# Kernel optimization log

Measured on AMD Instinct MI355X. Metric: run time of the kernel, lower is better.

## Reference

```python
import jax, jax.numpy as jnp
import numpy as np
from jax import lax


def setup_inputs() -> dict:
    key = jax.random.key(0)
    k1, k2, k3 = jax.random.split(key, 3)
    B, H, W_, C = 2, 384, 1280, 3
    F = 32
    return {
        "xl": jax.random.normal(k1, (B, H, W_, C), dtype=jnp.float32),
        "xr": jax.random.normal(k2, (B, H, W_, C), dtype=jnp.float32),
        "W": jax.random.normal(k3, (3, 3, C, F), dtype=jnp.float32) * 0.1,
        "b": jnp.zeros((F,), dtype=jnp.float32),
        "num_disparity": 96,
    }


def _features(x, W, b):
    # stand-in for the pretrained backbone: 3x3 stride-2 conv + relu (channels_last)
    f = lax.conv_general_dilated(x, W, window_strides=(2, 2), padding="SAME",
                                 dimension_numbers=("NHWC", "HWIO", "NHWC"))
    return jax.nn.relu(f + b)


def reference(xl, xr, W, b, num_disparity):
    D = num_disparity
    x = jnp.concatenate([xl, xr], axis=0)            # [2B,H,W,3]
    f = _features(x, W, b)                            # [2B,H/2,W/2,F]
    f = jax.image.resize(f, (f.shape[0], f.shape[1] * 2, f.shape[2] * 2, f.shape[3]),
                         method="bilinear")          # [2B,H,W,F]
    fl, fr = jnp.split(f, 2, axis=0)                  # each [B,H,W,F]

    # plane-sweep cost volume: sum over channels of squared diff vs width-rolled right features
    def step(_, d):
        cost_d = jnp.sum((fl - jnp.roll(fr, d, axis=2)) ** 2, axis=-1)  # [B,H,W]
        return None, cost_d

    _, cost = lax.scan(step, None, jnp.arange(D))     # [D,B,H,W]

    s = -177.0 * cost / jnp.max(cost, axis=0, keepdims=True)
    w = jax.nn.softmax(s, axis=0)
    disp_idx = jnp.arange(D, dtype=w.dtype)[:, None, None, None]
    return jnp.sum(disp_idx * w, axis=0)              # [B,H,W]
```

## Files before the change

### kernel.cpp

```cpp
#include <hip/hip_runtime.h>
#include <cstddef>

typedef _Float16 h2    __attribute__((ext_vector_type(2)));
typedef _Float16 half8 __attribute__((ext_vector_type(8)));
typedef float    f32x4 __attribute__((ext_vector_type(4)));
typedef float    f32x2 __attribute__((ext_vector_type(2)));

#define CH    192
#define CWID  640
#define IMG_H 384
#define IMG_W 1280
#define TW    128
#define GR    224
#define RAWC  179
#define RAWP  192

__device__ __forceinline__ float fastrcp(float x) {
#if __has_builtin(__builtin_amdgcn_rcpf)
  return __builtin_amdgcn_rcpf(x);
#else
  return 1.0f / x;
#endif
}
__device__ __forceinline__ float fastexp2(float x) {
#if __has_builtin(__builtin_amdgcn_exp2f)
  return __builtin_amdgcn_exp2f(x);
#else
  return exp2f(x);
#endif
}
__device__ __forceinline__ f32x2 xsw16(float x) {
#if __has_builtin(__builtin_amdgcn_permlane16_swap)
  auto r = __builtin_amdgcn_permlane16_swap(__float_as_uint(x), __float_as_uint(x), false, false);
  f32x2 o; o.x = __uint_as_float(r[0]); o.y = __uint_as_float(r[1]); return o;
#else
  f32x2 o; o.x = x;
  o.y = __uint_as_float((unsigned)__builtin_amdgcn_ds_swizzle((int)__float_as_uint(x), 0x401F));
  return o;
#endif
}
__device__ __forceinline__ f32x2 xsw32(float x) {
#if __has_builtin(__builtin_amdgcn_permlane32_swap)
  auto r = __builtin_amdgcn_permlane32_swap(__float_as_uint(x), __float_as_uint(x), false, false);
  f32x2 o; o.x = __uint_as_float(r[0]); o.y = __uint_as_float(r[1]); return o;
#else
  const int bpa = ((threadIdx.x & 63) ^ 32) << 2;
  f32x2 o; o.x = x;
  o.y = __uint_as_float((unsigned)__builtin_amdgcn_ds_bpermute(bpa, (int)__float_as_uint(x)));
  return o;
#endif
}
__device__ __forceinline__ f32x2 pkadd(f32x2 a, f32x2 b) {
  f32x2 d; asm("v_pk_add_f32 %0, %1, %2" : "=v"(d) : "v"(a), "v"(b)); return d;
}
__device__ __forceinline__ f32x2 pkfma(f32x2 a, f32x2 b, f32x2 c) {
  f32x2 d; asm("v_pk_fma_f32 %0, %1, %2, %3" : "=v"(d) : "v"(a), "v"(b), "v"(c)); return d;
}
__device__ __forceinline__ float min3f(float a, float b, float c) {
  float d; asm("v_min3_f32 %0, %1, %2, %3" : "=v"(d) : "v"(a), "v"(b), "v"(c)); return d;
}
__device__ __forceinline__ float max3f(float a, float b, float c) {
  float d; asm("v_max3_f32 %0, %1, %2, %3" : "=v"(d) : "v"(a), "v"(b), "v"(c)); return d;
}
__device__ __forceinline__ f32x2 lo2(f32x4 v) { f32x2 r; r.x = v.x; r.y = v.y; return r; }
__device__ __forceinline__ f32x2 hi2(f32x4 v) { f32x2 r; r.x = v.z; r.y = v.w; return r; }

__global__ __launch_bounds__(256)
void conv_relu_kernel(const float* __restrict__ xl, const float* __restrict__ xr,
                      const float* __restrict__ Wt, const float* __restrict__ bias,
                      _Float16* __restrict__ Fc) {
  __shared__ float wl[864];
  __shared__ float bl[32];
  const int tid = threadIdx.x;
  for (int t = tid; t < 864; t += 256) wl[t] = Wt[t];
  if (tid < 32) bl[tid] = bias[tid];
  __syncthreads();

  const int g  = blockIdx.x * 256 + tid;
  const int ow = g % CWID;
  const int t2 = g / CWID;
  const int oh = t2 % CH;
  const int bb = t2 / CH;
  const float* src = (bb < 2) ? (xl + (size_t)bb * IMG_H * IMG_W * 3)
                              : (xr + (size_t)(bb - 2) * IMG_H * IMG_W * 3);
  float acc[32];
  #pragma unroll
  for (int c = 0; c < 32; ++c) acc[c] = bl[c];

  #pragma unroll
  for (int kh = 0; kh < 3; ++kh) {
    const int ir = oh * 2 + kh;
    if (ir >= IMG_H) continue;
    #pragma unroll
    for (int kw = 0; kw < 3; ++kw) {
      const int ic = ow * 2 + kw;
      if (ic >= IMG_W) continue;
      const float* px = src + ((size_t)ir * IMG_W + ic) * 3;
      #pragma unroll
      for (int ci = 0; ci < 3; ++ci) {
        const float v = px[ci];
        const float* wp = &wl[((kh * 3 + kw) * 3 + ci) * 32];
        #pragma unroll
        for (int c8 = 0; c8 < 8; ++c8) {
          const float4 w4 = *(const float4*)(wp + c8 * 4);
          acc[c8 * 4 + 0] = fmaf(v, w4.x, acc[c8 * 4 + 0]);
          acc[c8 * 4 + 1] = fmaf(v, w4.y, acc[c8 * 4 + 1]);
          acc[c8 * 4 + 2] = fmaf(v, w4.z, acc[c8 * 4 + 2]);
          acc[c8 * 4 + 3] = fmaf(v, w4.w, acc[c8 * 4 + 3]);
        }
      }
    }
  }
  _Float16 hv[32];
  #pragma unroll
  for (int c = 0; c < 32; ++c) hv[c] = (_Float16)fmaxf(acc[c], 0.f);
  half8* dst = (half8*)(Fc + (size_t)g * 32);
  #pragma unroll
  for (int q = 0; q < 4; ++q) {
    half8 o;
    #pragma unroll
    for (int e = 0; e < 8; ++e) o[e] = hv[q * 8 + e];
    dst[q] = o;
  }
}

__global__ __launch_bounds__(256, 4)
void disparity_mfma_kernel(const _Float16* __restrict__ Fc, float* __restrict__ out) {
  __shared__ alignas(16) _Float16 raw[RAWP * 16];
  __shared__ alignas(16) _Float16 flH[8 * 512];
  __shared__ alignas(16) _Float16 gH[14 * 512];
  __shared__ alignas(16) float As[TW];
  __shared__ alignas(16) float Bs[GR];

  const int tid = threadIdx.x;
  const int w0  = blockIdx.x * TW;
  const int h   = blockIdx.y;
  const int bz  = blockIdx.z;

  const int hk = h >> 1;
  int r0, r1; float wv0;
  if (h & 1) { r0 = hk; r1 = (hk + 1 > CH - 1) ? CH - 1 : hk + 1; wv0 = 0.75f; }
  else       { r0 = (hk - 1 < 0) ? 0 : hk - 1; r1 = hk;           wv0 = 0.25f; }
  const half8 w0v = (half8)(_Float16)wv0;
  const half8 w1v = (half8)(_Float16)(1.0f - wv0);

  const int vbaseL = (w0 >> 1) + 639;
  const int vbaseR = (w0 >> 1) + 592;

  char* const rawB = (char*)raw;

  const char* const bL0 = (const char*)(Fc + ((size_t)bz * CH + r0) * CWID * 32);
  const char* const bL1 = (const char*)(Fc + ((size_t)bz * CH + r1) * CWID * 32);
  const char* const bR0 = (const char*)(Fc + ((size_t)(bz + 2) * CH + r0) * CWID * 32);
  const char* const bR1 = (const char*)(Fc + ((size_t)(bz + 2) * CH + r1) * CWID * 32);

  const _Float16 h75 = (_Float16)0.75f, h25 = (_Float16)0.25f;
  int a_r0off, a_s0, a_r1off, a_s1, a_swz; half8 a_h0, a_h1; char* a_dst;
  int b_r0off, b_s0, b_r1off, b_s1, b_swz; half8 b_h0, b_h1; char* b_dst;
  {
    const int row = tid;
    const bool isfl = row < TW;
    const int r  = isfl ? row : row - TW;
    const int uv = isfl ? (w0 + r) : (w0 - 95 + r);
    const int uact = uv < 0 ? uv + IMG_W : (uv >= IMG_W ? uv - IMG_W : uv);
    const int up = uv + IMG_W;
    const int vm0 = (up - 1) >> 1;
    int t0 = vm0 - (isfl ? vbaseL : (vbaseR - 66));
    int t1 = t0 + 1;
    if (uact == 0)         t0 = t1;
    if (uact == IMG_W - 1) t1 = t0;
    a_h0 = (half8)((up & 1) ? h75 : h25);
    a_h1 = (half8)((up & 1) ? h25 : h75);
    a_r0off = t0 * 32; a_s0 = (t0 & 1) << 4;
    a_r1off = t1 * 32; a_s1 = (t1 & 1) << 4;
    a_swz = (r >> 1) & 3;
    a_dst = (char*)(isfl ? flH : gH) + (r >> 4) * 1024 + (r & 15) * 64;
  }
  {
    const int row = tid + 256;
    const int r  = row - TW;
    const int uv = w0 - 95 + r;
    const int uact = uv < 0 ? uv + IMG_W : (uv >= IMG_W ? uv - IMG_W : uv);
    const int up = uv + IMG_W;
    const int vm0 = (up - 1) >> 1;
    int t0 = vm0 - (vbaseR - 66);
    int t1 = t0 + 1;
    if (uact == 0)         t0 = t1;
    if (uact == IMG_W - 1) t1 = t0;
    b_h0 = (half8)((up & 1) ? h75 : h25);
    b_h1 = (half8)((up & 1) ? h25 : h75);
    b_r0off = t0 * 32; b_s0 = (t0 & 1) << 4;
    b_r1off = t1 * 32; b_s1 = (t1 & 1) << 4;
    b_swz = (r >> 1) & 3;
    b_dst = (char*)gH + (r >> 4) * 1024 + (r & 15) * 64;
  }

  float sA = 0.f, sB = 0.f;
  #pragma unroll
  for (int half = 0; half < 2; ++half) {
    #pragma unroll
    for (int it = 0; it < 2; ++it) {
      const int task = tid + it * 256;
      if (it == 0 || tid < 128) {
        const int t    = task >> 1;
        const int cpos = task & 1;
        const int tc   = (t > RAWC - 1) ? RAWC - 1 : t;
        const bool isfl = tc < 66;
        int v = isfl ? (vbaseL + tc) : (vbaseR + tc - 66);
        v -= (v >= 640) ? 640 : 0;
        v -= (v >= 640) ? 640 : 0;
        const char* p0 = isfl ? bL0 : bR0;
        const char* p1 = isfl ? bL1 : bR1;
        const int off = (v << 6) + ((half * 2 + cpos) << 4);
        const half8 a0 = *(const half8*)(p0 + off);
        const half8 a1 = *(const half8*)(p1 + off);
        const half8 vv = a0 * w0v + a1 * w1v;
        *(half8*)(rawB + t * 32 + ((cpos ^ (t & 1)) << 4)) = vv;
      }
    }
    __syncthreads();

    #pragma unroll
    for (int cpos = 0; cpos < 2; ++cpos) {
      const int c16 = half * 2 + cpos;
      const int cb  = cpos << 4;
      {
        const half8 a = *(const half8*)(rawB + a_r0off + (cb ^ a_s0));
        const half8 b = *(const half8*)(rawB + a_r1off + (cb ^ a_s1));
        const half8 v = a * a_h0 + b * a_h1;
        #pragma unroll
        for (int e = 0; e < 4; ++e) {
          h2 pe = {v[2 * e], v[2 * e + 1]};
#if __has_builtin(__builtin_amdgcn_fdot2)
          sA = __builtin_amdgcn_fdot2(pe, pe, sA, false);
#else
          sA += (float)pe[0] * (float)pe[0] + (float)pe[1] * (float)pe[1];
#endif
        }
        *(half8*)(a_dst + ((c16 ^ a_swz) << 4)) = v;
      }
      if (tid < TW + GR - 256) {
        const half8 a = *(const half8*)(rawB + b_r0off + (cb ^ b_s0));
        const half8 b = *(const half8*)(rawB + b_r1off + (cb ^ b_s1));
        const half8 v = a * b_h0 + b * b_h1;
        #pragma unroll
        for (int e = 0; e < 4; ++e) {
          h2 pe = {v[2 * e], v[2 * e + 1]};
#if __has_builtin(__builtin_amdgcn_fdot2)
          sB = __builtin_amdgcn_fdot2(pe, pe, sB, false);
#else
          sB += (float)pe[0] * (float)pe[0] + (float)pe[1] * (float)pe[1];
#endif
        }
        *(half8*)(b_dst + ((c16 ^ b_swz) << 4)) = v;
      }
    }
    __syncthreads();
  }
  if (tid < TW) As[tid] = sA; else Bs[tid - TW] = sA;
  if (tid < TW + GR - 256) Bs[tid + 256 - TW] = sB;
  __syncthreads();

  const int lane = tid & 63;
  const int wid  = tid >> 6;
  const int n  = lane & 15;
  const int gq = lane >> 4;
  const int foffB = n * 64 + ((gq ^ ((n >> 1) & 3)) << 4);
  const float Cbase = (float)(95 - 4 * gq + n);

  const int mmb = gq * 4;
  const bool s0 = (mmb + 0) >= n, s1 = (mmb + 1) >= n;
  const bool s2 = (mmb + 2) >= n, s3 = (mmb + 3) >= n;
  const float kf0 = s0 ? 0.f : 96.f;
  const float kf1 = s1 ? 1.f : 97.f;
  const float kf2 = s2 ? 2.f : 98.f;
  const float kf3 = s3 ? 3.f : 99.f;

  #pragma unroll
  for (int pp = 0; pp < 2; ++pp) {
    const int p = wid * 2 + pp;
    const half8 bfrag = *(const half8*)((const char*)flH + p * 1024 + foffB);
    f32x4 acc[7];
    #pragma unroll
    for (int dq = 0; dq < 7; ++dq) {
      const half8 afrag = *(const half8*)((const char*)gH + (p + dq) * 1024 + foffB);
      f32x4 z = {0.f, 0.f, 0.f, 0.f};
      acc[dq] = __builtin_amdgcn_mfma_f32_16x16x32_f16(afrag, bfrag, z, 0, 0, 0);
    }

    const float Ai = As[p * 16 + n];
    const f32x4 b40 = *(const f32x4*)(&Bs[p * 16 + mmb]);
    const f32x4 b46 = *(const f32x4*)(&Bs[(p + 6) * 16 + mmb]);
    const float cm0 = fmaf(-2.f, s0 ? acc[0].x : acc[6].x, Ai + (s0 ? b40.x : b46.x));
    const float cm1 = fmaf(-2.f, s1 ? acc[0].y : acc[6].y, Ai + (s1 ? b40.y : b46.y));
    const float cm2 = fmaf(-2.f, s2 ? acc[0].z : acc[6].z, Ai + (s2 ? b40.z : b46.z));
    const float cm3 = fmaf(-2.f, s3 ? acc[0].w : acc[6].w, Ai + (s3 ? b40.w : b46.w));
    float mn = min3f(fminf(cm0, cm1), cm2, cm3);
    float mx = max3f(fmaxf(cm0, cm1), cm2, cm3);

    f32x2 AiP; AiP.x = Ai; AiP.y = Ai;
    f32x2 m2P; m2P.x = -2.f; m2P.y = -2.f;
    #pragma unroll
    for (int dq = 1; dq < 6; ++dq) {
      const f32x4 b4 = *(const f32x4*)(&Bs[(p + dq) * 16 + mmb]);
      const f32x2 c01 = pkfma(m2P, lo2(acc[dq]), pkadd(AiP, lo2(b4)));
      const f32x2 c23 = pkfma(m2P, hi2(acc[dq]), pkadd(AiP, hi2(b4)));
      mn = min3f(mn, c01.x, c01.y);
      mn = min3f(mn, c23.x, c23.y);
      mx = max3f(mx, c01.x, c01.y);
      mx = max3f(mx, c23.x, c23.y);
      acc[dq].x = c01.x; acc[dq].y = c01.y;
      acc[dq].z = c23.x; acc[dq].w = c23.y;
    }
    f32x2 t;
    t = xsw16(mn); mn = fminf(t.x, t.y);
    t = xsw32(mn); mn = fminf(t.x, t.y);
    t = xsw16(mx); mx = fmaxf(t.x, t.y);
    t = xsw32(mx); mx = fmaxf(t.x, t.y);

    const float ralpha = 177.0f * 1.4426950408889634f * fastrcp(mx);
    const float na   = -ralpha;
    const float base = ralpha * mn;
    f32x2 naP;   naP.x = na;   naP.y = na;
    f32x2 baseP; baseP.x = base; baseP.y = base;
    const float w0_ = fastexp2(fmaf(na, cm0, base));
    const float w1_ = fastexp2(fmaf(na, cm1, base));
    const float w2_ = fastexp2(fmaf(na, cm2, base));
    const float w3_ = fastexp2(fmaf(na, cm3, base));
    float sw0 = w0_, sw1 = w1_, sw2 = w2_, sw3 = w3_;
    float sk0 = kf0 * w0_;
    float sk1 = kf1 * w1_;
    float sk2 = kf2 * w2_;
    float sk3 = kf3 * w3_;
    #pragma unroll
    for (int dq = 1; dq < 6; ++dq) {
      const f32x2 g01 = pkfma(naP, lo2(acc[dq]), baseP);
      const f32x2 g23 = pkfma(naP, hi2(acc[dq]), baseP);
      const float u0 = fastexp2(g01.x);
      const float u1 = fastexp2(g01.y);
      const float u2 = fastexp2(g23.x);
      const float u3 = fastexp2(g23.y);
      sw0 += u0; sw1 += u1; sw2 += u2; sw3 += u3;
      sk0 = fmaf((float)(16 * dq + 0), u0, sk0);
      sk1 = fmaf((float)(16 * dq + 1), u1, sk1);
      sk2 = fmaf((float)(16 * dq + 2), u2, sk2);
      sk3 = fmaf((float)(16 * dq + 3), u3, sk3);
    }
    float sw  = (sw0 + sw1) + (sw2 + sw3);
    float skw = (sk0 + sk1) + (sk2 + sk3);
    float sdw = fmaf(Cbase, sw, -skw);
    t = xsw16(sw);  sw  = t.x + t.y;
    t = xsw16(sdw); sdw = t.x + t.y;
    t = xsw32(sw);  sw  = t.x + t.y;
    t = xsw32(sdw); sdw = t.x + t.y;
    if (gq == 0)
      out[((size_t)bz * IMG_H + h) * IMG_W + w0 + p * 16 + n] = sdw * fastrcp(sw);
  }
}

extern "C" void kernel_launch(void* const* d_in, const int* in_sizes, int n_in,
                              void* d_out, int out_size, void* d_ws, size_t ws_size,
                              hipStream_t stream) {
  (void)in_sizes; (void)n_in; (void)out_size; (void)ws_size;
  const float* xl   = (const float*)d_in[0];
  const float* xr   = (const float*)d_in[1];
  const float* Wt   = (const float*)d_in[2];
  const float* bias = (const float*)d_in[3];
  _Float16* Fc = (_Float16*)d_ws;
  float* out = (float*)d_out;

  hipLaunchKernelGGL(conv_relu_kernel, dim3(1920), dim3(256), 0, stream,
                     xl, xr, Wt, bias, Fc);
  hipLaunchKernelGGL(disparity_mfma_kernel, dim3(IMG_W / TW, IMG_H, 2), dim3(256), 0, stream,
                     Fc, out);
}
```

Baseline: 73.60 us.

## Move backbone conv to split-fp16 MFMA with LDS-staged input tiles

The scalar per-pixel 3x3 stride-2 conv is replaced by a tiled kernel. It stages five input rows in LDS, builds an im2col patch matrix with K=27 padded to 32, and computes it with 16x16x32 fp16 MFMAs. Precision is kept with a hi/lo fp16 split (three MFMAs per tile). The disparity kernel also drops the per-row Ai addition from every cost candidate and folds it into the max normalisation instead, since min and argmin shift uniformly. This costs extra LDS, swizzled layouts and split-precision work for the conv.

```diff
diff --git a/kernel.cpp b/kernel.cpp
--- a/kernel.cpp
+++ b/kernel.cpp
@@ -2,6 +2,7 @@
 #include <cstddef>
 
 typedef _Float16 h2    __attribute__((ext_vector_type(2)));
+typedef _Float16 half4 __attribute__((ext_vector_type(4)));
 typedef _Float16 half8 __attribute__((ext_vector_type(8)));
 typedef float    f32x4 __attribute__((ext_vector_type(4)));
 typedef float    f32x2 __attribute__((ext_vector_type(2)));
@@ -50,9 +51,6 @@
   return o;
 #endif
 }
-__device__ __forceinline__ f32x2 pkadd(f32x2 a, f32x2 b) {
-  f32x2 d; asm("v_pk_add_f32 %0, %1, %2" : "=v"(d) : "v"(a), "v"(b)); return d;
-}
 __device__ __forceinline__ f32x2 pkfma(f32x2 a, f32x2 b, f32x2 c) {
   f32x2 d; asm("v_pk_fma_f32 %0, %1, %2, %3" : "=v"(d) : "v"(a), "v"(b), "v"(c)); return d;
 }
@@ -66,61 +64,143 @@
 __device__ __forceinline__ f32x2 hi2(f32x4 v) { f32x2 r; r.x = v.z; r.y = v.w; return r; }
 
 __global__ __launch_bounds__(256)
-void conv_relu_kernel(const float* __restrict__ xl, const float* __restrict__ xr,
+void conv_mfma_kernel(const float* __restrict__ xl, const float* __restrict__ xr,
                       const float* __restrict__ Wt, const float* __restrict__ bias,
                       _Float16* __restrict__ Fc) {
-  __shared__ float wl[864];
+  __shared__ alignas(16) float lin[5 * 776];
+  __shared__ alignas(16) _Float16 Ph[256 * 32];
+  __shared__ alignas(16) _Float16 Pl[256 * 32];
+  __shared__ alignas(16) _Float16 Wh[32 * 32];
+  __shared__ alignas(16) _Float16 Wl[32 * 32];
   __shared__ float bl[32];
+
   const int tid = threadIdx.x;
-  for (int t = tid; t < 864; t += 256) wl[t] = Wt[t];
+  const int bx = blockIdx.x;
+  const int by = blockIdx.y;
+  const int bb = blockIdx.z;
+  const float* src = (bb < 2) ? (xl + (size_t)bb * (IMG_H * IMG_W * 3))
+                              : (xr + (size_t)(bb - 2) * (IMG_H * IMG_W * 3));
+
+  const int fbase = bx * 768;
+  #pragma unroll
+  for (int r = 0; r < 5; ++r) {
+    const int ir = by * 4 + r;
+    const float* grow = src + (size_t)ir * 3840;
+    #pragma unroll
+    for (int j = 0; j < 2; ++j) {
+      const int pr = tid + j * 256;
+      if (pr < 388) {
+        const int fo = fbase + 2 * pr;
+        float2 v; v.x = 0.f; v.y = 0.f;
+        if (ir < IMG_H && fo < 3840) v = *(const float2*)(grow + fo);
+        *(float2*)(&lin[r * 776 + 2 * pr]) = v;
+      }
+    }
+  }
+  if (tid < 128) {
+    const int ch = tid >> 2, ck = tid & 3;
+    half8 hv, lv;
+    #pragma unroll
+    for (int e = 0; e < 8; ++e) {
+      const int k = ck * 8 + e;
+      const float v = (k < 27) ? Wt[k * 32 + ch] : 0.f;
+      const _Float16 hh = (_Float16)v;
+      hv[e] = hh;
+      lv[e] = (_Float16)(v - (float)hh);
+    }
+    const int off = ch * 32 + ((ck ^ ((ch >> 1) & 3)) << 3);
+    *(half8*)(&Wh[off]) = hv;
+    *(half8*)(&Wl[off]) = lv;
+  }
   if (tid < 32) bl[tid] = bias[tid];
   __syncthreads();
 
-  const int g  = blockIdx.x * 256 + tid;
-  const int ow = g % CWID;
-  const int t2 = g / CWID;
-  const int oh = t2 % CH;
-  const int bb = t2 / CH;
-  const float* src = (bb < 2) ? (xl + (size_t)bb * IMG_H * IMG_W * 3)
-                              : (xr + (size_t)(bb - 2) * IMG_H * IMG_W * 3);
-  float acc[32];
+  {
+    const int dow = tid & 127;
+    const int doh = tid >> 7;
+    const int pb = tid * 32;
+    const int sz = (tid >> 1) & 3;
+    auto emit = [&](int c, float v0, float v1, float v2, float v3,
+                    float v4, float v5, float v6, float v7) {
+      const float vv[8] = {v0, v1, v2, v3, v4, v5, v6, v7};
+      half8 hv, lv;
+      #pragma unroll
+      for (int e = 0; e < 8; ++e) {
+        const _Float16 hh = (_Float16)vv[e];
+        hv[e] = hh;
+        lv[e] = (_Float16)(vv[e] - (float)hh);
+      }
+      const int off = pb + ((c ^ sz) << 3);
+      *(half8*)(&Ph[off]) = hv;
+      *(half8*)(&Pl[off]) = lv;
+    };
+    const int lb0 = (doh * 2) * 776 + 6 * dow;
+    const float2 a0 = *(const float2*)(&lin[lb0 + 0]);
+    const float2 a1 = *(const float2*)(&lin[lb0 + 2]);
+    const float2 a2 = *(const float2*)(&lin[lb0 + 4]);
+    const float2 a3 = *(const float2*)(&lin[lb0 + 6]);
+    const float  a8 = lin[lb0 + 8];
+    emit(0, a0.x, a0.y, a1.x, a1.y, a2.x, a2.y, a3.x, a3.y);
+    const int lb1 = lb0 + 776;
+    const float2 b0 = *(const float2*)(&lin[lb1 + 0]);
+    const float2 b1 = *(const float2*)(&lin[lb1 + 2]);
+    const float2 b2 = *(const float2*)(&lin[lb1 + 4]);
+    const float2 b3 = *(const float2*)(&lin[lb1 + 6]);
+    const float  b8 = lin[lb1 + 8];
+    emit(1, a8, b0.x, b0.y, b1.x, b1.y, b2.x, b2.y, b3.x);
+    const int lb2 = lb0 + 1552;
+    const float2 d0 = *(const float2*)(&lin[lb2 + 0]);
+    const float2 d1 = *(const float2*)(&lin[lb2 + 2]);
+    const float2 d2 = *(const float2*)(&lin[lb2 + 4]);
+    const float2 d3 = *(const float2*)(&lin[lb2 + 6]);
+    const float  d8 = lin[lb2 + 8];
+    emit(2, b3.y, b8, d0.x, d0.y, d1.x, d1.y, d2.x, d2.y);
+    emit(3, d3.x, d3.y, d8, 0.f, 0.f, 0.f, 0.f, 0.f);
+  }
+  __syncthreads();
+
+  const int lane = tid & 63, wv = tid >> 6;
+  const int n  = lane & 15;
+  const int gq = lane >> 4;
+  const int fs = (gq ^ ((n >> 1) & 3)) << 3;
+  const half8 wh0 = *(const half8*)(&Wh[n * 32 + fs]);
+  const half8 wl0 = *(const half8*)(&Wl[n * 32 + fs]);
+  const half8 wh1 = *(const half8*)(&Wh[(16 + n) * 32 + fs]);
+  const half8 wl1 = *(const half8*)(&Wl[(16 + n) * 32 + fs]);
+  const float bb0 = bl[gq * 4 + 0], bb1 = bl[gq * 4 + 1];
+  const float bb2 = bl[gq * 4 + 2], bb3 = bl[gq * 4 + 3];
+  const float bc0 = bl[16 + gq * 4 + 0], bc1 = bl[16 + gq * 4 + 1];
+  const float bc2 = bl[16 + gq * 4 + 2], bc3 = bl[16 + gq * 4 + 3];
+
   #pragma unroll
-  for (int c = 0; c < 32; ++c) acc[c] = bl[c];
-
-  #pragma unroll
-  for (int kh = 0; kh < 3; ++kh) {
-    const int ir = oh * 2 + kh;
-    if (ir >= IMG_H) continue;
-    #pragma unroll
-    for (int kw = 0; kw < 3; ++kw) {
-      const int ic = ow * 2 + kw;
-      if (ic >= IMG_W) continue;
-      const float* px = src + ((size_t)ir * IMG_W + ic) * 3;
-      #pragma unroll
-      for (int ci = 0; ci < 3; ++ci) {
-        const float v = px[ci];
-        const float* wp = &wl[((kh * 3 + kw) * 3 + ci) * 32];
-        #pragma unroll
-        for (int c8 = 0; c8 < 8; ++c8) {
-          const float4 w4 = *(const float4*)(wp + c8 * 4);
-          acc[c8 * 4 + 0] = fmaf(v, w4.x, acc[c8 * 4 + 0]);
-          acc[c8 * 4 + 1] = fmaf(v, w4.y, acc[c8 * 4 + 1]);
-          acc[c8 * 4 + 2] = fmaf(v, w4.z, acc[c8 * 4 + 2]);
-          acc[c8 * 4 + 3] = fmaf(v, w4.w, acc[c8 * 4 + 3]);
-        }
-      }
-    }
-  }
-  _Float16 hv[32];
-  #pragma unroll
-  for (int c = 0; c < 32; ++c) hv[c] = (_Float16)fmaxf(acc[c], 0.f);
-  half8* dst = (half8*)(Fc + (size_t)g * 32);
-  #pragma unroll
-  for (int q = 0; q < 4; ++q) {
-    half8 o;
-    #pragma unroll
-    for (int e = 0; e < 8; ++e) o[e] = hv[q * 8 + e];
-    dst[q] = o;
+  for (int t = 0; t < 4; ++t) {
+    const int px = wv * 64 + t * 16 + n;
+    const int poff = px * 32 + fs;
+    const half8 ph = *(const half8*)(&Ph[poff]);
+    const half8 pl = *(const half8*)(&Pl[poff]);
+    f32x4 z0 = {0.f, 0.f, 0.f, 0.f};
+    z0 = __builtin_amdgcn_mfma_f32_16x16x32_f16(wh0, pl, z0, 0, 0, 0);
+    z0 = __builtin_amdgcn_mfma_f32_16x16x32_f16(wl0, ph, z0, 0, 0, 0);
+    z0 = __builtin_amdgcn_mfma_f32_16x16x32_f16(wh0, ph, z0, 0, 0, 0);
+    f32x4 z1 = {0.f, 0.f, 0.f, 0.f};
+    z1 = __builtin_amdgcn_mfma_f32_16x16x32_f16(wh1, pl, z1, 0, 0, 0);
+    z1 = __builtin_amdgcn_mfma_f32_16x16x32_f16(wl1, ph, z1, 0, 0, 0);
+    z1 = __builtin_amdgcn_mfma_f32_16x16x32_f16(wh1, ph, z1, 0, 0, 0);
+
+    const int ow = bx * 128 + (px & 127);
+    const int oh = by * 2 + (px >> 7);
+    _Float16* fp = Fc + ((size_t)(bb * CH + oh) * CWID + ow) * 32 + gq * 4;
+    half4 o0, o1;
+    o0[0] = (_Float16)fmaxf(z0[0] + bb0, 0.f);
+    o0[1] = (_Float16)fmaxf(z0[1] + bb1, 0.f);
+    o0[2] = (_Float16)fmaxf(z0[2] + bb2, 0.f);
+    o0[3] = (_Float16)fmaxf(z0[3] + bb3, 0.f);
+    o1[0] = (_Float16)fmaxf(z1[0] + bc0, 0.f);
+    o1[1] = (_Float16)fmaxf(z1[1] + bc1, 0.f);
+    o1[2] = (_Float16)fmaxf(z1[2] + bc2, 0.f);
+    o1[3] = (_Float16)fmaxf(z1[3] + bc3, 0.f);
+    *(half4*)(fp)      = o0;
+    *(half4*)(fp + 16) = o1;
   }
 }
 
@@ -291,20 +371,19 @@
     const float Ai = As[p * 16 + n];
     const f32x4 b40 = *(const f32x4*)(&Bs[p * 16 + mmb]);
     const f32x4 b46 = *(const f32x4*)(&Bs[(p + 6) * 16 + mmb]);
-    const float cm0 = fmaf(-2.f, s0 ? acc[0].x : acc[6].x, Ai + (s0 ? b40.x : b46.x));
-    const float cm1 = fmaf(-2.f, s1 ? acc[0].y : acc[6].y, Ai + (s1 ? b40.y : b46.y));
-    const float cm2 = fmaf(-2.f, s2 ? acc[0].z : acc[6].z, Ai + (s2 ? b40.z : b46.z));
-    const float cm3 = fmaf(-2.f, s3 ? acc[0].w : acc[6].w, Ai + (s3 ? b40.w : b46.w));
+    const float cm0 = fmaf(-2.f, s0 ? acc[0].x : acc[6].x, s0 ? b40.x : b46.x);
+    const float cm1 = fmaf(-2.f, s1 ? acc[0].y : acc[6].y, s1 ? b40.y : b46.y);
+    const float cm2 = fmaf(-2.f, s2 ? acc[0].z : acc[6].z, s2 ? b40.z : b46.z);
+    const float cm3 = fmaf(-2.f, s3 ? acc[0].w : acc[6].w, s3 ? b40.w : b46.w);
     float mn = min3f(fminf(cm0, cm1), cm2, cm3);
     float mx = max3f(fmaxf(cm0, cm1), cm2, cm3);
 
-    f32x2 AiP; AiP.x = Ai; AiP.y = Ai;
     f32x2 m2P; m2P.x = -2.f; m2P.y = -2.f;
     #pragma unroll
     for (int dq = 1; dq < 6; ++dq) {
       const f32x4 b4 = *(const f32x4*)(&Bs[(p + dq) * 16 + mmb]);
-      const f32x2 c01 = pkfma(m2P, lo2(acc[dq]), pkadd(AiP, lo2(b4)));
-      const f32x2 c23 = pkfma(m2P, hi2(acc[dq]), pkadd(AiP, hi2(b4)));
+      const f32x2 c01 = pkfma(m2P, lo2(acc[dq]), lo2(b4));
+      const f32x2 c23 = pkfma(m2P, hi2(acc[dq]), hi2(b4));
       mn = min3f(mn, c01.x, c01.y);
       mn = min3f(mn, c23.x, c23.y);
       mx = max3f(mx, c01.x, c01.y);
@@ -318,7 +397,7 @@
     t = xsw16(mx); mx = fmaxf(t.x, t.y);
     t = xsw32(mx); mx = fmaxf(t.x, t.y);
 
-    const float ralpha = 177.0f * 1.4426950408889634f * fastrcp(mx);
+    const float ralpha = 177.0f * 1.4426950408889634f * fastrcp(Ai + mx);
     const float na   = -ralpha;
     const float base = ralpha * mn;
     f32x2 naP;   naP.x = na;   naP.y = na;
@@ -369,7 +448,7 @@
   _Float16* Fc = (_Float16*)d_ws;
   float* out = (float*)d_out;
 
-  hipLaunchKernelGGL(conv_relu_kernel, dim3(1920), dim3(256), 0, stream,
+  hipLaunchKernelGGL(conv_mfma_kernel, dim3(5, 96, 4), dim3(256), 0, stream,
                      xl, xr, Wt, bias, Fc);
   hipLaunchKernelGGL(disparity_mfma_kernel, dim3(IMG_W / TW, IMG_H, 2), dim3(256), 0, stream,
                      Fc, out);
```

Measured after the change: 71.34 us. 1.03x faster.
